# Optimization experiments

Hardware: AMD Instinct MI355X
Metric: run time of the kernel (lower is better)

Reference implementation:

```python
import jax, jax.numpy as jnp
import numpy as np
import math

B, S, D, H = 4, 2048, 1024, 16
DH = D // H  # 64
DFF = 4 * D
EPS = 1e-5


def layer_norm(x, g, b):
    mu = jnp.mean(x, axis=-1, keepdims=True)
    var = jnp.mean(jnp.square(x - mu), axis=-1, keepdims=True)
    return (x - mu) * jax.lax.rsqrt(var + EPS) * g + b


def apply_rope(xq, xk, freqs_cis):
    # xq, xk: [B, S, H, DH]; freqs_cis: [S, DH//2, 2] (cos, sin)
    cos = freqs_cis[None, :, None, :, 0]  # [1, S, 1, DH//2]
    sin = freqs_cis[None, :, None, :, 1]

    def rot(t):
        tr = t.reshape(*t.shape[:-1], DH // 2, 2)
        t0, t1 = tr[..., 0], tr[..., 1]
        o0 = t0 * cos - t1 * sin
        o1 = t0 * sin + t1 * cos
        return jnp.stack([o0, o1], axis=-1).reshape(t.shape)

    return rot(xq), rot(xk)


def setup_inputs() -> dict:
    key = jax.random.key(0)
    ks = jax.random.split(key, 12)
    x = jax.random.normal(ks[0], (B, S, D), dtype=jnp.float32)
    # rotary frequencies (theta = 10000), stored as (cos, sin)
    inv = 1.0 / (10000.0 ** (np.arange(0, DH, 2, dtype=np.float32) / DH))
    t = np.arange(S, dtype=np.float32)
    ang = np.outer(t, inv)  # [S, DH//2]
    freqs_cis = jnp.asarray(np.stack([np.cos(ang), np.sin(ang)], axis=-1))
    s = 1.0 / math.sqrt(D)
    sf = 1.0 / math.sqrt(DFF)
    return {
        "x": x,
        "freqs_cis": freqs_cis,
        "wq": jax.random.normal(ks[1], (D, D), dtype=jnp.float32) * s,
        "wk": jax.random.normal(ks[2], (D, D), dtype=jnp.float32) * s,
        "wv": jax.random.normal(ks[3], (D, D), dtype=jnp.float32) * s,
        "w_proj": jax.random.normal(ks[4], (D, D), dtype=jnp.float32) * s,
        "b_proj": jnp.zeros((D,), dtype=jnp.float32),
        "w_ff1": jax.random.normal(ks[5], (D, DFF), dtype=jnp.float32) * s,
        "b_ff1": jnp.zeros((DFF,), dtype=jnp.float32),
        "w_ff2": jax.random.normal(ks[6], (DFF, D), dtype=jnp.float32) * sf,
        "b_ff2": jnp.zeros((D,), dtype=jnp.float32),
        "ln1_g": jnp.ones((D,), dtype=jnp.float32),
        "ln1_b": jnp.zeros((D,), dtype=jnp.float32),
        "ln2_g": jnp.ones((D,), dtype=jnp.float32),
        "ln2_b": jnp.zeros((D,), dtype=jnp.float32),
    }


def reference(x, freqs_cis, wq, wk, wv, w_proj, b_proj, w_ff1, b_ff1, w_ff2,
              b_ff2, ln1_g, ln1_b, ln2_g, ln2_b):
    # --- attention block (pre-norm) ---
    h = layer_norm(x, ln1_g, ln1_b)
    xq = (h @ wq).reshape(B, S, H, DH)
    xk = (h @ wk).reshape(B, S, H, DH)
    xv = (h @ wv).reshape(B, S, H, DH)
    xq, xk = apply_rope(xq, xk, freqs_cis)
    # [B, H, S, S]
    att = jnp.einsum("bqhd,bkhd->bhqk", xq, xk) / math.sqrt(DH)
    att = jax.nn.softmax(att, axis=-1)
    out = jnp.einsum("bhqk,bkhd->bqhd", att, xv).reshape(B, S, D)
    x = x + out @ w_proj + b_proj
    # --- feed-forward block (pre-norm, GELU) ---
    h2 = layer_norm(x, ln2_g, ln2_b)
    ff = jax.nn.gelu(h2 @ w_ff1 + b_ff1, approximate=False) @ w_ff2 + b_ff2
    return x + ff
```

## Files before the change

### kernel.cpp

```cpp
#include <hip/hip_runtime.h>
#include <hip/hip_bf16.h>


#define Bb_ 4
#define Ss_ 2048
#define Dd_ 1024
#define Hh_ 16
#define DFF_ 4096

typedef __bf16 bf16x8 __attribute__((ext_vector_type(8)));
typedef float f32x4 __attribute__((ext_vector_type(4)));

static __device__ __forceinline__ unsigned short f2bf(float f) {
  union { float f; unsigned u; } v; v.f = f;
  unsigned r = v.u + 0x7FFF + ((v.u >> 16) & 1);
  return (unsigned short)(r >> 16);
}
static __device__ __forceinline__ float bf2f(unsigned short h) {
  union { unsigned u; float f; } v; v.u = ((unsigned)h) << 16;
  return v.f;
}
static __device__ __forceinline__ unsigned cvt_pk_bf16(float lo, float hi) {
  unsigned r;
  asm("v_cvt_pk_bf16_f32 %0, %1, %2" : "=v"(r) : "v"(lo), "v"(hi));
  return r;
}

static __device__ __forceinline__ void gl16(const unsigned short* g, void* l) {
  __builtin_amdgcn_global_load_lds(
      (const __attribute__((address_space(1))) void*)g,
      (__attribute__((address_space(3))) void*)l, 16, 0, 0);
}

__global__ __launch_bounds__(256) void ln_kernel(
    const float* __restrict__ x, const float* __restrict__ g,
    const float* __restrict__ bb, unsigned short* __restrict__ out)
{
  const int row = blockIdx.x;
  const int t = threadIdx.x;
  const float4 v = reinterpret_cast<const float4*>(x + (size_t)row * Dd_)[t];
  float s = v.x + v.y + v.z + v.w;
  float ss = v.x*v.x + v.y*v.y + v.z*v.z + v.w*v.w;
  #pragma unroll
  for (int o = 32; o; o >>= 1) { s += __shfl_down(s, o); ss += __shfl_down(ss, o); }
  __shared__ float red[8];
  if ((t & 63) == 0) { red[t >> 6] = s; red[4 + (t >> 6)] = ss; }
  __syncthreads();
  s = red[0] + red[1] + red[2] + red[3];
  ss = red[4] + red[5] + red[6] + red[7];
  const float mean = s * (1.f / Dd_);
  const float var = ss * (1.f / Dd_) - mean * mean;
  const float inv = rsqrtf(var + 1e-5f);
  const float4 gv = reinterpret_cast<const float4*>(g)[t];
  const float4 bv = reinterpret_cast<const float4*>(bb)[t];
  ushort4 o4;
  o4.x = f2bf((v.x - mean) * inv * gv.x + bv.x);
  o4.y = f2bf((v.y - mean) * inv * gv.y + bv.y);
  o4.z = f2bf((v.z - mean) * inv * gv.z + bv.z);
  o4.w = f2bf((v.w - mean) * inv * gv.w + bv.w);
  reinterpret_cast<ushort4*>(out + (size_t)row * Dd_)[t] = o4;
}

__global__ __launch_bounds__(256) void tconv_kernel(
    const float* __restrict__ src, unsigned short* __restrict__ dst, int K, int N)
{
  __shared__ float tile[32][33];
  const int bx = blockIdx.x, by = blockIdx.y;
  const int tx = threadIdx.x & 31, ty = threadIdx.x >> 5;
  #pragma unroll
  for (int i = 0; i < 4; i++)
    tile[ty + i * 8][tx] = src[(size_t)(by * 32 + ty + i * 8) * N + bx * 32 + tx];
  __syncthreads();
  #pragma unroll
  for (int i = 0; i < 4; i++)
    dst[(size_t)(bx * 32 + ty + i * 8) * K + by * 32 + tx] = f2bf(tile[tx][ty + i * 8]);
}

template<int MODE>
__global__ __launch_bounds__(256) void gemm_kernel(
    const unsigned short* __restrict__ A,
    const unsigned short* __restrict__ BT,
    int K, int nbn, int N,
    const float* __restrict__ bias,
    const float* __restrict__ resid,
    void* __restrict__ out,
    const float* __restrict__ fcp,
    void* __restrict__ out2)
{
  __shared__ unsigned short As[2][128 * 64];
  __shared__ unsigned short Bs[2][128 * 64];
  const int t = threadIdx.x;

  const int nwg = gridDim.x;
  const int id = blockIdx.x;
  const int sid = (id & 7) * (nwg >> 3) + (id >> 3);
  const int bm = sid / nbn, bn = sid % nbn;

  const int w = t >> 6, lane = t & 63;
  const int lq = lane >> 4, lr = lane & 15;
  const int wm = (w >> 1) * 64, wn = (w & 1) * 64;
  const int srow = t >> 3, sg8 = t & 7;
  const int sw8 = sg8 ^ (srow & 7);

  const unsigned short* ag = A  + (size_t)(bm * 128 + srow) * K + sw8 * 8;
  const unsigned short* bg = BT + (size_t)(bn * 128 + srow) * K + sw8 * 8;

  char* AsB = (char*)As;
  char* BsB = (char*)Bs;
  const int csw = (lr & 7) * 8;
  int aoffB[2], boffB[2];
  aoffB[0] = (wm + lr) * 128 + 2 * ((lq * 8) ^ csw);
  aoffB[1] = (wm + lr) * 128 + 2 * ((32 + lq * 8) ^ csw);
  boffB[0] = (wn + lr) * 128 + 2 * ((lq * 8) ^ csw);
  boffB[1] = (wn + lr) * 128 + 2 * ((32 + lq * 8) ^ csw);
  const int sdstB = (srow * 64 + sg8 * 8) * 2;

  f32x4 acc[4][4] = {};
  const int nt = K >> 6;

#define STAGE7(BUF)                                                          \
  {                                                                          \
    _Pragma("unroll")                                                        \
    for (int i_ = 0; i_ < 4; i_++) {                                         \
      gl16(ag + (size_t)i_ * 32 * K, AsB + (BUF) * 16384 + sdstB + i_ * 4096); \
      gl16(bg + (size_t)i_ * 32 * K, BsB + (BUF) * 16384 + sdstB + i_ * 4096); \
    }                                                                        \
    ag += 64; bg += 64;                                                      \
  }

#define COMPUTE7(BUF)                                                        \
  {                                                                          \
    __builtin_amdgcn_s_setprio(1);                                           \
    _Pragma("unroll")                                                        \
    for (int kc_ = 0; kc_ < 2; kc_++) {                                      \
      bf16x8 af[4], bfr[4];                                                  \
      _Pragma("unroll")                                                      \
      for (int i_ = 0; i_ < 4; i_++) {                                       \
        af[i_]  = *reinterpret_cast<const bf16x8*>(AsB + (BUF) * 16384 + aoffB[kc_] + i_ * 2048); \
        bfr[i_] = *reinterpret_cast<const bf16x8*>(BsB + (BUF) * 16384 + boffB[kc_] + i_ * 2048); \
      }                                                                      \
      _Pragma("unroll")                                                      \
      for (int i_ = 0; i_ < 4; i_++)                                         \
        _Pragma("unroll")                                                    \
        for (int j_ = 0; j_ < 4; j_++)                                       \
          acc[i_][j_] = __builtin_amdgcn_mfma_f32_16x16x32_bf16(af[i_], bfr[j_], acc[i_][j_], 0, 0, 0); \
    }                                                                        \
    __builtin_amdgcn_s_setprio(0);                                           \
  }

  STAGE7(0);
  __syncthreads();
  for (int t0 = 0; t0 < nt; t0 += 2) {
    STAGE7(1);
    COMPUTE7(0);
    __syncthreads();
    if (t0 + 2 < nt) STAGE7(0);
    COMPUTE7(1);
    __syncthreads();
  }
#undef STAGE7
#undef COMPUTE7

  const int growbase = bm * 128 + wm + lq * 4;
  const int gcolbase = bn * 128 + wn + lr;

  if (MODE == 0) {
    if (bn < 16) {
      const float sgn = (lr & 1) ? 1.f : -1.f;
      #pragma unroll
      for (int j = 0; j < 4; j++) {
        const int col = gcolbase + j * 16;
        const int ip = (col & 63) & ~1;
        #pragma unroll
        for (int i = 0; i < 4; i++) {
          #pragma unroll
          for (int r = 0; r < 4; r++) {
            const int grow = growbase + i * 16 + r;
            const int s = grow & (Ss_ - 1);
            const float2 cs = *reinterpret_cast<const float2*>(fcp + (size_t)s * 64 + ip);
            const float v = acc[i][j][r];
            const float p = __shfl_xor(v, 1);
            const float o = v * cs.x + sgn * p * cs.y;
            ((unsigned short*)out)[(size_t)grow * N + col] = f2bf(o);
          }
        }
      }
    } else {
      #pragma unroll
      for (int j = 0; j < 4; j++) {
        const int vcol = gcolbase + j * 16 - 2048;
        const int h = vcol >> 6, d = vcol & 63;
        #pragma unroll
        for (int i = 0; i < 4; i++) {
          const int g0 = growbase + i * 16;
          const int b = g0 >> 11, s0 = g0 & (Ss_ - 1);
          ushort4 o4;
          o4.x = f2bf(acc[i][j][0]);
          o4.y = f2bf(acc[i][j][1]);
          o4.z = f2bf(acc[i][j][2]);
          o4.w = f2bf(acc[i][j][3]);
          unsigned short* vr = (unsigned short*)out2 +
              ((size_t)((b * 16 + h) * 64 + d)) * Ss_ + s0;
          *reinterpret_cast<ushort4*>(vr) = o4;
        }
      }
    }
  } else {
    #pragma unroll
    for (int j = 0; j < 4; j++) {
      const int col = gcolbase + j * 16;
      const float bj = bias[col];
      #pragma unroll
      for (int i = 0; i < 4; i++) {
        #pragma unroll
        for (int r = 0; r < 4; r++) {
          const int grow = growbase + i * 16 + r;
          const float v = acc[i][j][r];
          if (MODE == 1 || MODE == 3) {
            ((float*)out)[(size_t)grow * N + col] = v + bj + resid[(size_t)grow * N + col];
          } else {
            const float u = v + bj;
            const float gel = 0.5f * u * (1.f + erff(u * 0.70710678118654752f));
            ((unsigned short*)out)[(size_t)grow * N + col] = f2bf(gel);
          }
        }
      }
    }
  }
}

__global__ __launch_bounds__(256) void attn_kernel(
    const unsigned short* __restrict__ qkv,
    const unsigned short* __restrict__ vt,
    unsigned short* __restrict__ attout)
{
  __shared__ unsigned short Ks[2][64 * 64];
  __shared__ unsigned short Vs[2][64 * 64];
  __shared__ unsigned short Ps[128 * 64];
  const int qt = blockIdx.x, h = blockIdx.y, b = blockIdx.z;
  const int t = threadIdx.x, w = t >> 6, lane = t & 63;
  const int lq = lane >> 4, lr = lane & 15;
  const int srow = t >> 3, sg8 = t & 7;

  const unsigned short* kg = qkv + (size_t)(b * Ss_) * 3072 + 1024 + h * 64;
  const unsigned short* vg = vt + (size_t)((b * 16 + h) * 64) * Ss_;

  bf16x8 aq[2][2];
  {
    const unsigned short* qg = qkv + (size_t)(b * Ss_ + qt * 128) * 3072 + h * 64;
    #pragma unroll
    for (int mt = 0; mt < 2; mt++)
      #pragma unroll
      for (int kc = 0; kc < 2; kc++)
        aq[mt][kc] = *reinterpret_cast<const bf16x8*>(
            qg + (size_t)(w * 32 + mt * 16 + lr) * 3072 + kc * 32 + lq * 8);
  }

  bf16x8 ones;
  #pragma unroll
  for (int j = 0; j < 8; j++) ones[j] = (__bf16)1.0f;

  f32x4 oacc[2][4] = {};
  f32x4 ssum[2] = {};

  const int g8s0 = sg8 ^ ((srow)      & 7);
  const int g8s1 = sg8 ^ ((srow + 32) & 7);

  {
    gl16(kg + (size_t)(srow)      * 3072 + g8s0 * 8, &Ks[0][(srow)      * 64 + sg8 * 8]);
    gl16(kg + (size_t)(srow + 32) * 3072 + g8s1 * 8, &Ks[0][(srow + 32) * 64 + sg8 * 8]);
    gl16(vg + (size_t)(srow)      * Ss_  + g8s0 * 8, &Vs[0][(srow)      * 64 + sg8 * 8]);
    gl16(vg + (size_t)(srow + 32) * Ss_  + g8s1 * 8, &Vs[0][(srow + 32) * 64 + sg8 * 8]);
  }
  __syncthreads();

  const float SC2 = 0.125f * 1.44269504088896f;

  for (int kt = 0; kt < Ss_ / 64; ++kt) {
    const int cur = kt & 1;
    if (kt < Ss_ / 64 - 1) {
      const int nb = cur ^ 1;
      const size_t ko = (size_t)((kt + 1) * 64);
      gl16(kg + (ko + srow)      * 3072 + g8s0 * 8, &Ks[nb][(srow)      * 64 + sg8 * 8]);
      gl16(kg + (ko + srow + 32) * 3072 + g8s1 * 8, &Ks[nb][(srow + 32) * 64 + sg8 * 8]);
      gl16(vg + (size_t)(srow)      * Ss_ + (kt + 1) * 64 + g8s0 * 8, &Vs[nb][(srow)      * 64 + sg8 * 8]);
      gl16(vg + (size_t)(srow + 32) * Ss_ + (kt + 1) * 64 + g8s1 * 8, &Vs[nb][(srow + 32) * 64 + sg8 * 8]);
    }

    f32x4 sacc[2][4] = {};
    #pragma unroll
    for (int kc = 0; kc < 2; kc++) {
      const int cofs = kc * 32 + lq * 8;
      const int swz = (lr & 7) * 8;
      bf16x8 kb[4];
      #pragma unroll
      for (int nf = 0; nf < 4; nf++)
        kb[nf] = *reinterpret_cast<const bf16x8*>(&Ks[cur][(nf * 16 + lr) * 64 + (cofs ^ swz)]);
      #pragma unroll
      for (int mt = 0; mt < 2; mt++)
        #pragma unroll
        for (int nf = 0; nf < 4; nf++)
          sacc[mt][nf] = __builtin_amdgcn_mfma_f32_16x16x32_bf16(kb[nf], aq[mt][kc], sacc[mt][nf], 0, 0, 0);
    }

    #pragma unroll
    for (int mt = 0; mt < 2; mt++) {
      const int qrow = w * 32 + mt * 16 + lr;
      char* prow = reinterpret_cast<char*>(Ps) + qrow * 128;
      const int sw = (lr & 7) << 4;
      #pragma unroll
      for (int nf = 0; nf < 4; nf++) {
        const float p0 = __builtin_amdgcn_exp2f(sacc[mt][nf][0] * SC2);
        const float p1 = __builtin_amdgcn_exp2f(sacc[mt][nf][1] * SC2);
        const float p2 = __builtin_amdgcn_exp2f(sacc[mt][nf][2] * SC2);
        const float p3 = __builtin_amdgcn_exp2f(sacc[mt][nf][3] * SC2);
        uint2 pw;
        pw.x = cvt_pk_bf16(p0, p1);
        pw.y = cvt_pk_bf16(p2, p3);
        *reinterpret_cast<uint2*>(prow + ((nf * 32 + lq * 8) ^ sw)) = pw;
      }
    }

    #pragma unroll
    for (int kc = 0; kc < 2; kc++) {
      const int cofs = kc * 32 + lq * 8;
      const int swz = (lr & 7) * 8;
      bf16x8 pa[2], vb[4];
      #pragma unroll
      for (int mt = 0; mt < 2; mt++) {
        const int qrow = w * 32 + mt * 16 + lr;
        pa[mt] = *reinterpret_cast<const bf16x8*>(
            reinterpret_cast<const char*>(Ps) + qrow * 128 + ((kc * 64 + lq * 16) ^ ((lr & 7) << 4)));
      }
      #pragma unroll
      for (int mt = 0; mt < 2; mt++)
        ssum[mt] = __builtin_amdgcn_mfma_f32_16x16x32_bf16(pa[mt], ones, ssum[mt], 0, 0, 0);
      #pragma unroll
      for (int nf = 0; nf < 4; nf++)
        vb[nf] = *reinterpret_cast<const bf16x8*>(&Vs[cur][(nf * 16 + lr) * 64 + (cofs ^ swz)]);
      #pragma unroll
      for (int mt = 0; mt < 2; mt++)
        #pragma unroll
        for (int nf = 0; nf < 4; nf++)
          oacc[mt][nf] = __builtin_amdgcn_mfma_f32_16x16x32_bf16(pa[mt], vb[nf], oacc[mt][nf], 0, 0, 0);
    }

    __syncthreads();
  }

  #pragma unroll
  for (int mt = 0; mt < 2; mt++) {
    #pragma unroll
    for (int r = 0; r < 4; r++) {
      const float inv = 1.f / ssum[mt][r];
      const int grow = b * Ss_ + qt * 128 + w * 32 + mt * 16 + lq * 4 + r;
      #pragma unroll
      for (int nf = 0; nf < 4; nf++)
        attout[(size_t)grow * Dd_ + h * 64 + nf * 16 + lr] = f2bf(oacc[mt][nf][r] * inv);
    }
  }
}

extern "C" void kernel_launch(void* const* d_in, const int* in_sizes, int n_in,
                              void* d_out, int out_size, void* d_ws, size_t ws_size,
                              hipStream_t stream) {
  const float* x      = (const float*)d_in[0];
  const float* fc     = (const float*)d_in[1];
  const float* wq     = (const float*)d_in[2];
  const float* wk     = (const float*)d_in[3];
  const float* wv     = (const float*)d_in[4];
  const float* w_proj = (const float*)d_in[5];
  const float* b_proj = (const float*)d_in[6];
  const float* w_ff1  = (const float*)d_in[7];
  const float* b_ff1  = (const float*)d_in[8];
  const float* w_ff2  = (const float*)d_in[9];
  const float* b_ff2  = (const float*)d_in[10];
  const float* ln1_g  = (const float*)d_in[11];
  const float* ln1_b  = (const float*)d_in[12];
  const float* ln2_g  = (const float*)d_in[13];
  const float* ln2_b  = (const float*)d_in[14];

  char* ws = (char*)d_ws;
  unsigned short* hb     = (unsigned short*)(ws);
  unsigned short* wqkvT  = (unsigned short*)(ws + 16777216ull);
  unsigned short* wprojT = (unsigned short*)(ws + 23068672ull);
  unsigned short* wff1T  = (unsigned short*)(ws + 25165824ull);
  unsigned short* wff2T  = (unsigned short*)(ws + 33554432ull);
  float*          x2     = (float*)(ws + 41943040ull);
  unsigned short* vtb    = (unsigned short*)(ws + 41943040ull);
  unsigned short* attoutb= (unsigned short*)(ws + 75497472ull);
  unsigned short* qkvb   = (unsigned short*)(ws + 92274688ull);
  unsigned short* ff1b   = qkvb;

  dim3 blk(256);

  tconv_kernel<<<dim3(32, 32), blk, 0, stream>>>(wq, wqkvT, 1024, 1024);
  tconv_kernel<<<dim3(32, 32), blk, 0, stream>>>(wk, wqkvT + 1024 * 1024, 1024, 1024);
  tconv_kernel<<<dim3(32, 32), blk, 0, stream>>>(wv, wqkvT + 2 * 1024 * 1024, 1024, 1024);
  tconv_kernel<<<dim3(32, 32), blk, 0, stream>>>(w_proj, wprojT, 1024, 1024);
  tconv_kernel<<<dim3(128, 32), blk, 0, stream>>>(w_ff1, wff1T, 1024, 4096);
  tconv_kernel<<<dim3(32, 128), blk, 0, stream>>>(w_ff2, wff2T, 4096, 1024);

  ln_kernel<<<8192, blk, 0, stream>>>(x, ln1_g, ln1_b, hb);
  gemm_kernel<0><<<1536, blk, 0, stream>>>(hb, wqkvT, 1024, 24, 3072, nullptr, nullptr, qkvb, fc, vtb);
  attn_kernel<<<dim3(16, 16, 4), blk, 0, stream>>>(qkvb, vtb, attoutb);
  gemm_kernel<1><<<512, blk, 0, stream>>>(attoutb, wprojT, 1024, 8, 1024, b_proj, x, x2, nullptr, nullptr);
  ln_kernel<<<8192, blk, 0, stream>>>(x2, ln2_g, ln2_b, hb);
  gemm_kernel<2><<<2048, blk, 0, stream>>>(hb, wff1T, 1024, 32, 4096, b_ff1, nullptr, ff1b, nullptr, nullptr);
  gemm_kernel<3><<<512, blk, 0, stream>>>(ff1b, wff2T, 4096, 8, 1024, b_ff2, x2, (float*)d_out, nullptr, nullptr);
}
```

Before: 421.1 us.

## Use wider 128x256 GEMM tiles for projection and FFN matmuls

Adds a new GEMM kernel with 128x256 output tiles, each wave computing 128x64 with 32 MFMA accumulators, and uses it for the output projection and both FFN GEMMs. This halves grid sizes and raises arithmetic intensity per tile to cut LDS and global traffic. The new kernel is single-buffered in LDS, unlike the double-buffered original, so load/compute overlap may suffer. Grids of 256 blocks for the proj and FF2 GEMMs may underfill the 256 CUs' occupancy, and heavy register use from 128 accumulator vectors may limit waves.

```diff
diff --git a/kernel.cpp b/kernel.cpp
--- a/kernel.cpp
+++ b/kernel.cpp
@@ -77,6 +77,98 @@
 }
 
 template<int MODE>
+__global__ __launch_bounds__(256) void gemmw_kernel(
+    const unsigned short* __restrict__ A,
+    const unsigned short* __restrict__ BT,
+    int K, int nbn, int N,
+    const float* __restrict__ bias,
+    const float* __restrict__ resid,
+    void* __restrict__ out)
+{
+  __shared__ __align__(16) unsigned short As[128 * 64];
+  __shared__ __align__(16) unsigned short Bs[256 * 64];
+  const int t = threadIdx.x;
+
+  const int nwg = gridDim.x;
+  const int id = blockIdx.x;
+  const int sid = (id & 7) * (nwg >> 3) + (id >> 3);
+  const int bm = sid / nbn, bn = sid % nbn;
+
+  const int wc = t >> 6, lane = t & 63;
+  const int lq = lane >> 4, lr = lane & 15;
+  const int srow8 = t >> 3, sg8 = t & 7;
+  const int sw8 = sg8 ^ (srow8 & 7);
+
+  const unsigned short* ag = A  + (size_t)(bm * 128 + srow8) * K + sw8 * 8;
+  const unsigned short* bg = BT + (size_t)(bn * 256 + srow8) * K + sw8 * 8;
+
+  char* AsB = (char*)As;
+  char* BsB = (char*)Bs;
+  const int csw = (lr & 7) * 8;
+  int aoffB[2], boffB[2];
+  aoffB[0] = lr * 128 + 2 * ((lq * 8) ^ csw);
+  aoffB[1] = lr * 128 + 2 * ((32 + lq * 8) ^ csw);
+  boffB[0] = (wc * 64 + lr) * 128 + 2 * ((lq * 8) ^ csw);
+  boffB[1] = (wc * 64 + lr) * 128 + 2 * ((32 + lq * 8) ^ csw);
+  const int sdstB = t * 16;
+
+  f32x4 acc[8][4] = {};
+  const int nt = K >> 6;
+
+  for (int t0 = 0; t0 < nt; ++t0) {
+    #pragma unroll
+    for (int i_ = 0; i_ < 4; i_++)
+      gl16(ag + (size_t)(i_ * 32) * K, AsB + sdstB + i_ * 4096);
+    #pragma unroll
+    for (int i_ = 0; i_ < 8; i_++)
+      gl16(bg + (size_t)(i_ * 32) * K, BsB + sdstB + i_ * 4096);
+    ag += 64; bg += 64;
+    __syncthreads();
+
+    __builtin_amdgcn_s_setprio(1);
+    #pragma unroll
+    for (int kc = 0; kc < 2; kc++) {
+      bf16x8 bf[4];
+      #pragma unroll
+      for (int j = 0; j < 4; j++)
+        bf[j] = *reinterpret_cast<const bf16x8*>(BsB + boffB[kc] + j * 2048);
+      #pragma unroll
+      for (int i = 0; i < 8; i++) {
+        const bf16x8 af = *reinterpret_cast<const bf16x8*>(AsB + aoffB[kc] + i * 2048);
+        #pragma unroll
+        for (int j = 0; j < 4; j++)
+          acc[i][j] = __builtin_amdgcn_mfma_f32_16x16x32_bf16(af, bf[j], acc[i][j], 0, 0, 0);
+      }
+    }
+    __builtin_amdgcn_s_setprio(0);
+    __syncthreads();
+  }
+
+  const int growbase = bm * 128 + lq * 4;
+  const int gcolbase = bn * 256 + wc * 64 + lr;
+  #pragma unroll
+  for (int j = 0; j < 4; j++) {
+    const int col = gcolbase + j * 16;
+    const float bj = bias[col];
+    #pragma unroll
+    for (int i = 0; i < 8; i++) {
+      #pragma unroll
+      for (int r = 0; r < 4; r++) {
+        const int grow = growbase + i * 16 + r;
+        const float v = acc[i][j][r];
+        if (MODE == 1 || MODE == 3) {
+          ((float*)out)[(size_t)grow * N + col] = v + bj + resid[(size_t)grow * N + col];
+        } else {
+          const float u = v + bj;
+          const float gel = 0.5f * u * (1.f + erff(u * 0.70710678118654752f));
+          ((unsigned short*)out)[(size_t)grow * N + col] = f2bf(gel);
+        }
+      }
+    }
+  }
+}
+
+template<int MODE>
 __global__ __launch_bounds__(256) void gemm_kernel(
     const unsigned short* __restrict__ A,
     const unsigned short* __restrict__ BT,
@@ -404,8 +496,8 @@
   ln_kernel<<<8192, blk, 0, stream>>>(x, ln1_g, ln1_b, hb);
   gemm_kernel<0><<<1536, blk, 0, stream>>>(hb, wqkvT, 1024, 24, 3072, nullptr, nullptr, qkvb, fc, vtb);
   attn_kernel<<<dim3(16, 16, 4), blk, 0, stream>>>(qkvb, vtb, attoutb);
-  gemm_kernel<1><<<512, blk, 0, stream>>>(attoutb, wprojT, 1024, 8, 1024, b_proj, x, x2, nullptr, nullptr);
+  gemmw_kernel<1><<<256, blk, 0, stream>>>(attoutb, wprojT, 1024, 4, 1024, b_proj, x, x2);
   ln_kernel<<<8192, blk, 0, stream>>>(x2, ln2_g, ln2_b, hb);
-  gemm_kernel<2><<<2048, blk, 0, stream>>>(hb, wff1T, 1024, 32, 4096, b_ff1, nullptr, ff1b, nullptr, nullptr);
-  gemm_kernel<3><<<512, blk, 0, stream>>>(ff1b, wff2T, 4096, 8, 1024, b_ff2, x2, (float*)d_out, nullptr, nullptr);
-}
+  gemmw_kernel<2><<<1024, blk, 0, stream>>>(hb, wff1T, 1024, 16, 4096, b_ff1, nullptr, ff1b);
+  gemmw_kernel<3><<<256, blk, 0, stream>>>(ff1b, wff2T, 4096, 4, 1024, b_ff2, x2, (float*)d_out);
+}
```

After: 581.3 us. +38.0%, slower.
